# Kernel tuning notes

Measured on AMD Instinct MI355X. Metric: run time of the kernel, lower is better.

The kernel has to match this reference:

```python
import math
import jax, jax.numpy as jnp
import numpy as np

B, C_IN, C_OUT, K, STYLE_DIM, H, W = 8, 512, 512, 3, 512, 64, 64
EPS = 1e-8

def setup_inputs() -> dict:
    key = jax.random.key(0)
    k1, k2, k3, k4 = jax.random.split(key, 4)
    inp = {
        "input": jax.random.normal(k1, (B, C_IN, H, W), dtype=jnp.float32),
        "style": jax.random.normal(k2, (B, STYLE_DIM), dtype=jnp.float32),
        # learned params
        "weight": jax.random.normal(k3, (1, C_OUT, C_IN, K, K), dtype=jnp.float32),
        "mod_weight": jax.random.normal(k4, (C_IN, STYLE_DIM), dtype=jnp.float32),  # EqualLinear weight (lr_mul=1)
        "mod_bias": jnp.ones((C_IN,), dtype=jnp.float32),  # bias_init=1
    }
    return inp

def reference(input, style, weight, mod_weight, mod_bias):
    batch, in_ch, h, w = input.shape
    out_ch, ksize = weight.shape[1], weight.shape[-1]
    # EqualLinear modulation: scale = 1/sqrt(style_dim), lr_mul = 1
    mod_scale = 1.0 / math.sqrt(mod_weight.shape[1])
    s = style @ (mod_weight * mod_scale).T + mod_bias  # [B, C_in]
    # modulate weights per sample
    conv_scale = 1.0 / math.sqrt(in_ch * ksize * ksize)
    wmod = conv_scale * weight * s[:, None, :, None, None]  # [B, O, C, k, k]
    # demodulate
    demod = jax.lax.rsqrt(jnp.sum(wmod * wmod, axis=(2, 3, 4)) + EPS)  # [B, O]
    wmod = wmod * demod[:, :, None, None, None]
    # grouped conv with groups = batch
    wflat = wmod.reshape(batch * out_ch, in_ch, ksize, ksize)
    xflat = input.reshape(1, batch * in_ch, h, w)
    pad = ksize // 2
    out = jax.lax.conv_general_dilated(
        xflat, wflat,
        window_strides=(1, 1),
        padding=[(pad, pad), (pad, pad)],
        dimension_numbers=("NCHW", "OIHW", "NCHW"),
        feature_group_count=batch,
    )
    return out.reshape(batch, out_ch, h, w)
```

## Files before the change

### kernel.cpp

```cpp
#include <hip/hip_runtime.h>


typedef __bf16 bf16x8 __attribute__((ext_vector_type(8)));
typedef float f32x16 __attribute__((ext_vector_type(16)));

#define AS1 __attribute__((address_space(1)))
#define AS3 __attribute__((address_space(3)))
#define SB __builtin_amdgcn_sched_barrier(0)

__device__ __forceinline__ unsigned short f2bf(float f) {
  union { float f; unsigned int u; } v; v.f = f;
  unsigned int u = v.u;
  return (unsigned short)((u + 0x7fffu + ((u >> 16) & 1u)) >> 16);
}

__device__ __forceinline__ float dot8(float4 a0, float4 a1, float4 b0, float4 b1) {
  return a0.x*b0.x + a0.y*b0.y + a0.z*b0.z + a0.w*b0.w +
         a1.x*b1.x + a1.y*b1.y + a1.z*b1.z + a1.w*b1.w;
}

__global__ __launch_bounds__(256) void k_mod(
    const float* __restrict__ style, const float* __restrict__ mw,
    const float* __restrict__ mb, float* __restrict__ s,
    float* __restrict__ zp) {
  if (blockIdx.x == 0) {
    zp[threadIdx.x] = 0.f; zp[256 + threadIdx.x] = 0.f;
    zp[512 + threadIdx.x] = 0.f; zp[768 + threadIdx.x] = 0.f;
  }
  int wv = blockIdx.x * 4 + (threadIdx.x >> 6);
  int lane = threadIdx.x & 63;
  int t0 = wv * 4;
#pragma unroll
  for (int j = 0; j < 4; ++j) {
    int t = t0 + j, b = t >> 9, c = t & 511;
    const float4* mp = (const float4*)(mw + (size_t)c * 512 + lane * 8);
    const float4* sp = (const float4*)(style + (size_t)b * 512 + lane * 8);
    float p = dot8(mp[0], mp[1], sp[0], sp[1]);
#pragma unroll
    for (int off = 32; off; off >>= 1) p += __shfl_xor(p, off);
    if (lane == 0) s[t] = p * 0.04419417382415922f + mb[c];
  }
}

__global__ __launch_bounds__(256) void k_wprep(
    const float* __restrict__ w, float* __restrict__ wsq,
    unsigned short* __restrict__ wbf) {
  __shared__ float wl[4608];
  int o = blockIdx.x;
  int t = threadIdx.x;
  const float* wp = w + (size_t)o * 4608;
  for (int i = t; i < 4608; i += 256) wl[i] = wp[i];
  __syncthreads();
  int c0 = t * 2;
  float q0 = 0.f, q1 = 0.f;
  unsigned int rr[9];
#pragma unroll
  for (int k = 0; k < 9; ++k) {
    float v0 = wl[c0 * 9 + k], v1 = wl[c0 * 9 + 9 + k];
    q0 += v0 * v0; q1 += v1 * v1;
    rr[k] = (unsigned int)f2bf(v0) | ((unsigned int)f2bf(v1) << 16);
  }
  *(float2*)&wsq[o * 512 + c0] = make_float2(q0, q1);
#pragma unroll
  for (int k = 0; k < 9; ++k)
    *(unsigned int*)&wbf[((size_t)k * 512 + o) * 512 + c0] = rr[k];
}

__global__ __launch_bounds__(256) void k_scale(
    const float* __restrict__ wsq, const float* __restrict__ s,
    float* __restrict__ scale) {
  int o = blockIdx.x * 4 + (threadIdx.x >> 6);
  int lane = threadIdx.x & 63;
  const float4* wp = (const float4*)(wsq + (size_t)o * 512 + lane * 8);
  float4 w0 = wp[0], w1 = wp[1];
  const float cs = 0.014731391274719739f;
#pragma unroll
  for (int b = 0; b < 8; ++b) {
    const float4* sp = (const float4*)(s + (size_t)b * 512 + lane * 8);
    float4 s0 = sp[0], s1 = sp[1];
    s0.x *= s0.x; s0.y *= s0.y; s0.z *= s0.z; s0.w *= s0.w;
    s1.x *= s1.x; s1.y *= s1.y; s1.z *= s1.z; s1.w *= s1.w;
    float p = dot8(w0, w1, s0, s1);
#pragma unroll
    for (int off = 32; off; off >>= 1) p += __shfl_xor(p, off);
    if (lane == 0) scale[b * 512 + o] = cs * rsqrtf(cs * cs * p + 1e-8f);
  }
}

__global__ void k_xt(const float* __restrict__ x, const float* __restrict__ s,
                     unsigned short* __restrict__ xt) {
  __shared__ __align__(16) unsigned short tile[64 * 65 * 8];
  int bid = blockIdx.x;
  int b = bid >> 6, y = bid & 63;
  int t = threadIdx.x;
  int co = t >> 3, xo = t & 7;
  const float* xbase = x + ((size_t)(b * 512 + co * 8) * 64 + y) * 64 + xo * 8;
  float4 v[8][2];
#pragma unroll
  for (int j = 0; j < 8; ++j) {
    v[j][0] = *(const float4*)(xbase + (size_t)j * 4096);
    v[j][1] = *(const float4*)(xbase + (size_t)j * 4096 + 4);
  }
  float sv[8];
#pragma unroll
  for (int j = 0; j < 8; ++j) sv[j] = s[b * 512 + co * 8 + j];
#pragma unroll
  for (int k = 0; k < 8; ++k) {
    unsigned short r[8];
#pragma unroll
    for (int j = 0; j < 8; ++j) {
      float f = (k < 4) ? ((const float*)&v[j][0])[k & 3]
                        : ((const float*)&v[j][1])[k & 3];
      r[j] = f2bf(f * sv[j]);
    }
    int xr = xo * 8 + k;
    int unit = xr * 65 + (co ^ xr);
    *(ulonglong2*)&tile[unit * 8] = *(ulonglong2*)r;
  }
  __syncthreads();
  unsigned short* obase = xt + ((size_t)(b * 64 + y) * 64) * 512;
#pragma unroll
  for (int i = 0; i < 8; ++i) {
    int unit_o = i * 512 + t;
    int xr = unit_o >> 6, cor = unit_o & 63;
    int unit = xr * 65 + (cor ^ xr);
    *(ulonglong2*)&obase[(size_t)unit_o * 8] = *(const ulonglong2*)&tile[unit * 8];
  }
}

#define XISS 20
#define WOFF_US 10240
#define BUFU    28672

__global__ __launch_bounds__(512, 2) void k_conv(
    const unsigned short* __restrict__ xt, const unsigned short* __restrict__ wbf,
    const float* __restrict__ scale, const float* __restrict__ zp,
    float* __restrict__ out) {
  __shared__ __align__(16) unsigned short lds[2 * BUFU];

  int bid = blockIdx.x;
  int b = bid & 7;
  int rest = bid >> 3;
  int ob = rest & 3;
  int rest2 = rest >> 2;
  int yg = rest2 & 3;
  int xg = rest2 >> 2;

  int tid = threadIdx.x;
  int wid = tid >> 6;
  int wo = wid & 1, wyy = wid >> 1;
  int lane = tid & 63, ln31 = lane & 31, hi = lane >> 5;
  int cls = (wid >> 2) & 1;

  const char* srcp[7];
  const char* xglob = (const char*)(xt + (size_t)b * 64 * 64 * 512);
#pragma unroll
  for (int i = 0; i < 7; ++i) {
    int is = wid + i * 8;
    const char* p;
    if (is < XISS) {
      int e = is * 64 + lane;
      int chunk = e / 612;
      int rem = e - chunk * 612;
      int row = rem / 34;
      int xi = rem - row * 34;
      int y = yg * 16 + row - 1, x = xg * 32 + xi - 1;
      bool ok = (chunk < 2) && (y >= 0) && (y < 64) && (x >= 0) && (x < 64);
      p = ok ? xglob + 2 * ((y * 64 + x) * 512 + chunk * 8) : (const char*)zp;
    } else {
      int e2 = (is - XISS) * 64 + lane;
      int chunk = e2 / 1152;
      int rem = e2 - chunk * 1152;
      int tap = rem >> 7, o = rem & 127;
      p = (const char*)wbf + 2 * ((tap * 512 + ob * 128 + o) * 512 + chunk * 8);
    }
    srcp[i] = p;
  }

  f32x16 acc[8];
#pragma unroll
  for (int i = 0; i < 8; ++i)
    acc[i] = (f32x16){0,0,0,0,0,0,0,0,0,0,0,0,0,0,0,0};

  auto STAGE = [&](int bufu) {
#pragma unroll
    for (int i = 0; i < 7; ++i) {
      __builtin_amdgcn_global_load_lds(
          (const AS1 void*)srcp[i],
          (AS3 void*)&lds[bufu + (wid + i * 8) * 512], 16, 0, 0);
      srcp[i] += 32;
    }
  };

  auto LOADK = [&](const unsigned short* Xbp, const unsigned short* Abp,
                   int kx, bf16x8* bv, bf16x8* av) {
#pragma unroll
    for (int rr = 0; rr < 6; ++rr)
      bv[rr] = *(const bf16x8*)&Xbp[(rr * 34 + kx) * 8];
#pragma unroll
    for (int ky = 0; ky < 3; ++ky) {
      av[ky * 2]     = *(const bf16x8*)&Abp[(ky * 3 + kx) * 1024];
      av[ky * 2 + 1] = *(const bf16x8*)&Abp[(ky * 3 + kx) * 1024 + 256];
    }
  };

  auto MFK = [&](const bf16x8* bv, const bf16x8* av) {
    __builtin_amdgcn_s_setprio(1);
#pragma unroll
    for (int ky = 0; ky < 3; ++ky) {
#pragma unroll
      for (int ry = 0; ry < 4; ++ry) {
        acc[ry] = __builtin_amdgcn_mfma_f32_32x32x16_bf16(
            av[ky * 2], bv[ry + ky], acc[ry], 0, 0, 0);
        acc[4 + ry] = __builtin_amdgcn_mfma_f32_32x32x16_bf16(
            av[ky * 2 + 1], bv[ry + ky], acc[4 + ry], 0, 0, 0);
      }
    }
    __builtin_amdgcn_s_setprio(0);
  };

  auto COMPUTE = [&](const unsigned short* Xbp, const unsigned short* Abp) {
    bf16x8 b0[6], a0[6], b1[6], a1[6];
    if (cls == 0) {
      LOADK(Xbp, Abp, 0, b0, a0); SB;
      MFK(b0, a0); SB;
      LOADK(Xbp, Abp, 1, b1, a1); SB;
      MFK(b1, a1); SB;
      LOADK(Xbp, Abp, 2, b0, a0); SB;
      MFK(b0, a0);
    } else {
      LOADK(Xbp, Abp, 0, b0, a0);
      LOADK(Xbp, Abp, 1, b1, a1); SB;
      MFK(b0, a0); SB;
      LOADK(Xbp, Abp, 2, b0, a0); SB;
      MFK(b1, a1); SB;
      MFK(b0, a0);
    }
  };

  const unsigned short* Xb0 = &lds[(hi * 612 + wyy * 4 * 34 + ln31) * 8];
  const unsigned short* Ab0 = &lds[WOFF_US + (hi * 1152 + wo * 64 + ln31) * 8];
  const unsigned short* Xb1 = Xb0 + BUFU;
  const unsigned short* Ab1 = Ab0 + BUFU;

  STAGE(0);
  asm volatile("s_waitcnt vmcnt(0) lgkmcnt(0)" ::: "memory");
  __builtin_amdgcn_s_barrier();
  SB;

#pragma unroll 1
  for (int t = 0; t < 16; ++t) {
    STAGE(BUFU);
    COMPUTE(Xb0, Ab0);
    asm volatile("s_waitcnt vmcnt(0) lgkmcnt(0)" ::: "memory");
    __builtin_amdgcn_s_barrier();
    SB;
    if (t < 15) STAGE(0);
    COMPUTE(Xb1, Ab1);
    asm volatile("s_waitcnt vmcnt(0) lgkmcnt(0)" ::: "memory");
    __builtin_amdgcn_s_barrier();
    SB;
  }

  const float* scp = scale + b * 512 + ob * 128 + wo * 64;
  float* op = out + (((size_t)(b * 512 + ob * 128 + wo * 64) * 64) +
                     yg * 16 + wyy * 4) * 64 + xg * 32 + ln31;
#pragma unroll
  for (int oh = 0; oh < 2; ++oh) {
#pragma unroll
    for (int ry = 0; ry < 4; ++ry) {
      const f32x16& A = acc[oh * 4 + ry];
#pragma unroll
      for (int reg = 0; reg < 16; ++reg) {
        int orow = (reg & 3) + 8 * (reg >> 2) + hi * 4;
        int ol = oh * 32 + orow;
        op[(size_t)ol * 4096 + ry * 64] = A[reg] * scp[ol];
      }
    }
  }
}

extern "C" void kernel_launch(void* const* d_in, const int* in_sizes, int n_in,
                              void* d_out, int out_size, void* d_ws, size_t ws_size,
                              hipStream_t stream) {
  const float* x     = (const float*)d_in[0];
  const float* style = (const float*)d_in[1];
  const float* w     = (const float*)d_in[2];
  const float* mw    = (const float*)d_in[3];
  const float* mb    = (const float*)d_in[4];
  float* out = (float*)d_out;

  char* ws = (char*)d_ws;
  float* zp    = (float*)ws;
  float* s     = (float*)(ws + 4096);
  float* scale = (float*)(ws + 20480);
  float* wsq   = (float*)(ws + 36864);
  unsigned short* wbf = (unsigned short*)(ws + 1085440);
  unsigned short* xt  = (unsigned short*)(ws + 5804032);

  k_mod  <<<256,  256, 0, stream>>>(style, mw, mb, s, zp);
  k_wprep<<<512,  256, 0, stream>>>(w, wsq, wbf);
  k_scale<<<128,  256, 0, stream>>>(wsq, s, scale);
  k_xt   <<<512,  512, 0, stream>>>(x, s, xt);
  k_conv <<<256,  512, 0, stream>>>(xt, wbf, scale, zp, out);
}
```

Before: 184.7 us.

## Load conv weights directly from global into registers with a 4-deep LDS pipeline

```diff
diff --git a/kernel.cpp b/kernel.cpp
--- a/kernel.cpp
+++ b/kernel.cpp
@@ -44,7 +44,7 @@
 
 __global__ __launch_bounds__(256) void k_wprep(
     const float* __restrict__ w, float* __restrict__ wsq,
-    unsigned short* __restrict__ wbf) {
+    unsigned short* __restrict__ wbf2) {
   __shared__ float wl[4608];
   int o = blockIdx.x;
   int t = threadIdx.x;
@@ -62,8 +62,11 @@
   }
   *(float2*)&wsq[o * 512 + c0] = make_float2(q0, q1);
 #pragma unroll
-  for (int k = 0; k < 9; ++k)
-    *(unsigned int*)&wbf[((size_t)k * 512 + o) * 512 + c0] = rr[k];
+  for (int k = 0; k < 9; ++k) {
+    size_t idx = ((size_t)(k * 32 + (c0 >> 4)) * 512 + o) * 16 +
+                 ((c0 >> 3) & 1) * 8 + (c0 & 7);
+    *(unsigned int*)&wbf2[idx] = rr[k];
+  }
 }
 
 __global__ __launch_bounds__(256) void k_scale(
@@ -129,14 +132,13 @@
 }
 
 #define XISS 20
-#define WOFF_US 10240
-#define BUFU    28672
+#define BUFU  12288
 
 __global__ __launch_bounds__(512, 2) void k_conv(
-    const unsigned short* __restrict__ xt, const unsigned short* __restrict__ wbf,
+    const unsigned short* __restrict__ xt, const unsigned short* __restrict__ wbf2,
     const float* __restrict__ scale, const float* __restrict__ zp,
     float* __restrict__ out) {
-  __shared__ __align__(16) unsigned short lds[2 * BUFU];
+  __shared__ __align__(16) unsigned short lds[4 * BUFU];
 
   int bid = blockIdx.x;
   int b = bid & 7;
@@ -150,14 +152,13 @@
   int wid = tid >> 6;
   int wo = wid & 1, wyy = wid >> 1;
   int lane = tid & 63, ln31 = lane & 31, hi = lane >> 5;
-  int cls = (wid >> 2) & 1;
-
-  const char* srcp[7];
+
+  const char* srcp[3];
   const char* xglob = (const char*)(xt + (size_t)b * 64 * 64 * 512);
 #pragma unroll
-  for (int i = 0; i < 7; ++i) {
+  for (int i = 0; i < 3; ++i) {
     int is = wid + i * 8;
-    const char* p;
+    const char* p = (const char*)zp;
     if (is < XISS) {
       int e = is * 64 + lane;
       int chunk = e / 612;
@@ -166,45 +167,47 @@
       int xi = rem - row * 34;
       int y = yg * 16 + row - 1, x = xg * 32 + xi - 1;
       bool ok = (chunk < 2) && (y >= 0) && (y < 64) && (x >= 0) && (x < 64);
-      p = ok ? xglob + 2 * ((y * 64 + x) * 512 + chunk * 8) : (const char*)zp;
-    } else {
-      int e2 = (is - XISS) * 64 + lane;
-      int chunk = e2 / 1152;
-      int rem = e2 - chunk * 1152;
-      int tap = rem >> 7, o = rem & 127;
-      p = (const char*)wbf + 2 * ((tap * 512 + ob * 128 + o) * 512 + chunk * 8);
+      if (ok) p = xglob + 2 * ((y * 64 + x) * 512 + chunk * 8);
     }
     srcp[i] = p;
   }
+
+  const char* aw0 = (const char*)wbf2 +
+      2 * (((size_t)(ob * 128 + wo * 64 + ln31)) * 16 + hi * 8);
+  const char* aw1 = aw0 + 1024;
 
   f32x16 acc[8];
 #pragma unroll
   for (int i = 0; i < 8; ++i)
     acc[i] = (f32x16){0,0,0,0,0,0,0,0,0,0,0,0,0,0,0,0};
 
-  auto STAGE = [&](int bufu) {
-#pragma unroll
-    for (int i = 0; i < 7; ++i) {
+  auto STAGE = [&](int bufu, bool real) {
+#pragma unroll
+    for (int i = 0; i < 3; ++i) {
+      const char* src = real ? srcp[i] : (const char*)zp;
       __builtin_amdgcn_global_load_lds(
-          (const AS1 void*)srcp[i],
+          (const AS1 void*)src,
           (AS3 void*)&lds[bufu + (wid + i * 8) * 512], 16, 0, 0);
       srcp[i] += 32;
     }
   };
 
-  auto LOADK = [&](const unsigned short* Xbp, const unsigned short* Abp,
-                   int kx, bf16x8* bv, bf16x8* av) {
+  auto LOADA = [&](int kx, int aoff, bf16x8* A) {
+#pragma unroll
+    for (int ky = 0; ky < 3; ++ky) {
+      int tap = ky * 3 + kx;
+      A[ky * 2]     = *(const bf16x8*)(aw0 + (size_t)tap * 524288 + aoff);
+      A[ky * 2 + 1] = *(const bf16x8*)(aw1 + (size_t)tap * 524288 + aoff);
+    }
+  };
+
+  auto LOADB = [&](const unsigned short* Xbp, int kx, bf16x8* bv) {
 #pragma unroll
     for (int rr = 0; rr < 6; ++rr)
       bv[rr] = *(const bf16x8*)&Xbp[(rr * 34 + kx) * 8];
-#pragma unroll
-    for (int ky = 0; ky < 3; ++ky) {
-      av[ky * 2]     = *(const bf16x8*)&Abp[(ky * 3 + kx) * 1024];
-      av[ky * 2 + 1] = *(const bf16x8*)&Abp[(ky * 3 + kx) * 1024 + 256];
-    }
-  };
-
-  auto MFK = [&](const bf16x8* bv, const bf16x8* av) {
+  };
+
+  auto MFK = [&](const bf16x8* av, const bf16x8* bv) {
     __builtin_amdgcn_s_setprio(1);
 #pragma unroll
     for (int ky = 0; ky < 3; ++ky) {
@@ -219,47 +222,47 @@
     __builtin_amdgcn_s_setprio(0);
   };
 
-  auto COMPUTE = [&](const unsigned short* Xbp, const unsigned short* Abp) {
-    bf16x8 b0[6], a0[6], b1[6], a1[6];
-    if (cls == 0) {
-      LOADK(Xbp, Abp, 0, b0, a0); SB;
-      MFK(b0, a0); SB;
-      LOADK(Xbp, Abp, 1, b1, a1); SB;
-      MFK(b1, a1); SB;
-      LOADK(Xbp, Abp, 2, b0, a0); SB;
-      MFK(b0, a0);
-    } else {
-      LOADK(Xbp, Abp, 0, b0, a0);
-      LOADK(Xbp, Abp, 1, b1, a1); SB;
-      MFK(b0, a0); SB;
-      LOADK(Xbp, Abp, 2, b0, a0); SB;
-      MFK(b1, a1); SB;
-      MFK(b0, a0);
-    }
-  };
-
-  const unsigned short* Xb0 = &lds[(hi * 612 + wyy * 4 * 34 + ln31) * 8];
-  const unsigned short* Ab0 = &lds[WOFF_US + (hi * 1152 + wo * 64 + ln31) * 8];
-  const unsigned short* Xb1 = Xb0 + BUFU;
-  const unsigned short* Ab1 = Ab0 + BUFU;
-
-  STAGE(0);
-  asm volatile("s_waitcnt vmcnt(0) lgkmcnt(0)" ::: "memory");
+  auto PHASE = [&](const unsigned short* Xbp, int stageBufU, bool real,
+                   bf16x8* Su, bf16x8* Sl, int aoff) {
+    bf16x8 bv[6];
+    LOADB(Xbp, 0, bv);
+    STAGE(stageBufU, real);
+    LOADA(1, aoff, Sl);
+    MFK(Su, bv);
+    LOADB(Xbp, 1, bv);
+    LOADA(2, aoff, Su);
+    MFK(Sl, bv);
+    LOADB(Xbp, 2, bv);
+    LOADA(0, aoff + 16384, Sl);
+    MFK(Su, bv);
+    asm volatile("s_waitcnt vmcnt(9)" ::: "memory");
+    __builtin_amdgcn_s_barrier();
+    SB;
+  };
+
+  const unsigned short* Xw = &lds[(hi * 612 + wyy * 136 + ln31) * 8];
+  const unsigned short* Xq0 = Xw;
+  const unsigned short* Xq1 = Xw + BUFU;
+  const unsigned short* Xq2 = Xw + 2 * BUFU;
+  const unsigned short* Xq3 = Xw + 3 * BUFU;
+
+  bf16x8 SA[6], SB_[6];
+
+  STAGE(0, true);
+  STAGE(BUFU, true);
+  LOADA(0, 0, SA);
+  asm volatile("s_waitcnt vmcnt(9)" ::: "memory");
   __builtin_amdgcn_s_barrier();
   SB;
 
+  int aoff = 0;
 #pragma unroll 1
-  for (int t = 0; t < 16; ++t) {
-    STAGE(BUFU);
-    COMPUTE(Xb0, Ab0);
-    asm volatile("s_waitcnt vmcnt(0) lgkmcnt(0)" ::: "memory");
-    __builtin_amdgcn_s_barrier();
-    SB;
-    if (t < 15) STAGE(0);
-    COMPUTE(Xb1, Ab1);
-    asm volatile("s_waitcnt vmcnt(0) lgkmcnt(0)" ::: "memory");
-    __builtin_amdgcn_s_barrier();
-    SB;
+  for (int t4 = 0; t4 < 8; ++t4) {
+    bool r = (t4 < 7);
+    PHASE(Xq0, 2 * BUFU, true, SA, SB_, aoff); aoff += 16384;
+    PHASE(Xq1, 3 * BUFU, true, SB_, SA, aoff); aoff += 16384;
+    PHASE(Xq2, 0,        r,    SA, SB_, aoff); aoff += 16384;
+    PHASE(Xq3, 1 * BUFU, r,    SB_, SA, aoff); aoff += 16384;
   }
 
   const float* scp = scale + b * 512 + ob * 128 + wo * 64;
@@ -295,12 +298,12 @@
   float* s     = (float*)(ws + 4096);
   float* scale = (float*)(ws + 20480);
   float* wsq   = (float*)(ws + 36864);
-  unsigned short* wbf = (unsigned short*)(ws + 1085440);
-  unsigned short* xt  = (unsigned short*)(ws + 5804032);
+  unsigned short* wbf2 = (unsigned short*)(ws + 1085440);
+  unsigned short* xt   = (unsigned short*)(ws + 5804032);
 
   k_mod  <<<256,  256, 0, stream>>>(style, mw, mb, s, zp);
-  k_wprep<<<512,  256, 0, stream>>>(w, wsq, wbf);
+  k_wprep<<<512,  256, 0, stream>>>(w, wsq, wbf2);
   k_scale<<<128,  256, 0, stream>>>(wsq, s, scale);
   k_xt   <<<512,  512, 0, stream>>>(x, s, xt);
-  k_conv <<<256,  512, 0, stream>>>(xt, wbf, scale, zp, out);
-}
+  k_conv <<<256,  512, 0, stream>>>(xt, wbf2, scale, zp, out);
+}
```

Measured after the change: 178.0 us. -3.7%, faster.

## Restructure conv K-loop into triple-buffered X and double-buffered W pipeline

Applied to the files above, without the earlier changes.

```diff
diff --git a/kernel.cpp b/kernel.cpp
--- a/kernel.cpp
+++ b/kernel.cpp
@@ -128,15 +128,17 @@
   }
 }
 
-#define XISS 20
-#define WOFF_US 10240
-#define BUFU    28672
+#define XS0 0
+#define XS1 12288
+#define XS2 24576
+#define WS0 36864
+#define WS1 55296
 
 __global__ __launch_bounds__(512, 2) void k_conv(
     const unsigned short* __restrict__ xt, const unsigned short* __restrict__ wbf,
     const float* __restrict__ scale, const float* __restrict__ zp,
     float* __restrict__ out) {
-  __shared__ __align__(16) unsigned short lds[2 * BUFU];
+  __shared__ __align__(16) unsigned short lds[73728];
 
   int bid = blockIdx.x;
   int b = bid & 7;
@@ -150,31 +152,36 @@
   int wid = tid >> 6;
   int wo = wid & 1, wyy = wid >> 1;
   int lane = tid & 63, ln31 = lane & 31, hi = lane >> 5;
-  int cls = (wid >> 2) & 1;
-
-  const char* srcp[7];
+
+  const char* wsrc[5];
+  const char* xsrc[3];
   const char* xglob = (const char*)(xt + (size_t)b * 64 * 64 * 512);
 #pragma unroll
-  for (int i = 0; i < 7; ++i) {
-    int is = wid + i * 8;
-    const char* p;
-    if (is < XISS) {
-      int e = is * 64 + lane;
-      int chunk = e / 612;
-      int rem = e - chunk * 612;
-      int row = rem / 34;
-      int xi = rem - row * 34;
-      int y = yg * 16 + row - 1, x = xg * 32 + xi - 1;
-      bool ok = (chunk < 2) && (y >= 0) && (y < 64) && (x >= 0) && (x < 64);
-      p = ok ? xglob + 2 * ((y * 64 + x) * 512 + chunk * 8) : (const char*)zp;
-    } else {
-      int e2 = (is - XISS) * 64 + lane;
+  for (int j = 0; j < 5; ++j) {
+    int is2 = wid + 24 + j * 8;
+    if (is2 < 60) {
+      int e2 = (is2 - 24) * 64 + lane;
       int chunk = e2 / 1152;
       int rem = e2 - chunk * 1152;
       int tap = rem >> 7, o = rem & 127;
-      p = (const char*)wbf + 2 * ((tap * 512 + ob * 128 + o) * 512 + chunk * 8);
-    }
-    srcp[i] = p;
+      wsrc[j] = (const char*)wbf +
+                2 * ((tap * 512 + ob * 128 + o) * 512 + chunk * 8);
+    } else {
+      wsrc[j] = (const char*)zp;
+    }
+  }
+#pragma unroll
+  for (int j = 0; j < 3; ++j) {
+    int is = wid + j * 8;
+    int e = is * 64 + lane;
+    int chunk = e / 612;
+    int rem = e - chunk * 612;
+    int row = rem / 34;
+    int xi = rem - row * 34;
+    int y = yg * 16 + row - 1, x = xg * 32 + xi - 1;
+    bool ok = (chunk < 2) && (y >= 0) && (y < 64) && (x >= 0) && (x < 64);
+    xsrc[j] = ok ? xglob + 2 * ((y * 64 + x) * 512 + chunk * 8)
+                 : (const char*)zp;
   }
 
   f32x16 acc[8];
@@ -182,29 +189,42 @@
   for (int i = 0; i < 8; ++i)
     acc[i] = (f32x16){0,0,0,0,0,0,0,0,0,0,0,0,0,0,0,0};
 
-  auto STAGE = [&](int bufu) {
-#pragma unroll
-    for (int i = 0; i < 7; ++i) {
+  auto stageW = [&](int j, int wsb) {
+    int is2 = wid + 24 + j * 8;
+    if (is2 < 60) {
       __builtin_amdgcn_global_load_lds(
-          (const AS1 void*)srcp[i],
-          (AS3 void*)&lds[bufu + (wid + i * 8) * 512], 16, 0, 0);
-      srcp[i] += 32;
+          (const AS1 void*)wsrc[j],
+          (AS3 void*)&lds[wsb + (is2 - 24) * 512], 16, 0, 0);
+      wsrc[j] += 32;
     }
   };
-
-  auto LOADK = [&](const unsigned short* Xbp, const unsigned short* Abp,
-                   int kx, bf16x8* bv, bf16x8* av) {
+  auto stageX = [&](int j, int xsb) {
+    __builtin_amdgcn_global_load_lds(
+        (const AS1 void*)xsrc[j],
+        (AS3 void*)&lds[xsb + (wid + j * 8) * 512], 16, 0, 0);
+    xsrc[j] += 32;
+  };
+
+  auto PHASE = [&](const unsigned short* Xr, const unsigned short* Wr, int kx,
+                   int sk, int sbase, bool sg, int wait) {
+    bf16x8 bv[6], av[6];
 #pragma unroll
     for (int rr = 0; rr < 6; ++rr)
-      bv[rr] = *(const bf16x8*)&Xbp[(rr * 34 + kx) * 8];
+      bv[rr] = *(const bf16x8*)&Xr[(rr * 34 + kx) * 8];
 #pragma unroll
     for (int ky = 0; ky < 3; ++ky) {
-      av[ky * 2]     = *(const bf16x8*)&Abp[(ky * 3 + kx) * 1024];
-      av[ky * 2 + 1] = *(const bf16x8*)&Abp[(ky * 3 + kx) * 1024 + 256];
-    }
-  };
-
-  auto MFK = [&](const bf16x8* bv, const bf16x8* av) {
+      av[ky * 2]     = *(const bf16x8*)&Wr[(ky * 3 + kx) * 1024];
+      av[ky * 2 + 1] = *(const bf16x8*)&Wr[(ky * 3 + kx) * 1024 + 256];
+    }
+    if (sg) {
+      if (sk == 0) { stageW(0, sbase); stageW(1, sbase); stageW(2, sbase); }
+      if (sk == 1) { stageW(3, sbase); stageW(4, sbase); }
+      if (sk == 2) { stageX(0, sbase); stageX(1, sbase); stageX(2, sbase); }
+    }
+    SB;
+    __builtin_amdgcn_s_barrier();
+    asm volatile("s_waitcnt lgkmcnt(0)" ::: "memory");
+    SB;
     __builtin_amdgcn_s_setprio(1);
 #pragma unroll
     for (int ky = 0; ky < 3; ++ky) {
@@ -217,50 +237,49 @@
       }
     }
     __builtin_amdgcn_s_setprio(0);
+    SB;
+    if (wait == 1) asm volatile("s_waitcnt vmcnt(3)" ::: "memory");
+    if (wait == 2) asm volatile("s_waitcnt vmcnt(0)" ::: "memory");
+    __builtin_amdgcn_s_barrier();
+    SB;
   };
 
-  auto COMPUTE = [&](const unsigned short* Xbp, const unsigned short* Abp) {
-    bf16x8 b0[6], a0[6], b1[6], a1[6];
-    if (cls == 0) {
-      LOADK(Xbp, Abp, 0, b0, a0); SB;
-      MFK(b0, a0); SB;
-      LOADK(Xbp, Abp, 1, b1, a1); SB;
-      MFK(b1, a1); SB;
-      LOADK(Xbp, Abp, 2, b0, a0); SB;
-      MFK(b0, a0);
-    } else {
-      LOADK(Xbp, Abp, 0, b0, a0);
-      LOADK(Xbp, Abp, 1, b1, a1); SB;
-      MFK(b0, a0); SB;
-      LOADK(Xbp, Abp, 2, b0, a0); SB;
-      MFK(b1, a1); SB;
-      MFK(b0, a0);
-    }
+  auto TILE = [&](const unsigned short* Xr, const unsigned short* Wr,
+                  int wsb, int xsb, bool sgW, bool sgX, int wcode) {
+    PHASE(Xr, Wr, 0, 0, wsb, sgW, 0);
+    PHASE(Xr, Wr, 1, 1, wsb, sgW, 0);
+    PHASE(Xr, Wr, 2, 2, xsb, sgX, wcode);
   };
 
-  const unsigned short* Xb0 = &lds[(hi * 612 + wyy * 4 * 34 + ln31) * 8];
-  const unsigned short* Ab0 = &lds[WOFF_US + (hi * 1152 + wo * 64 + ln31) * 8];
-  const unsigned short* Xb1 = Xb0 + BUFU;
-  const unsigned short* Ab1 = Ab0 + BUFU;
-
-  STAGE(0);
-  asm volatile("s_waitcnt vmcnt(0) lgkmcnt(0)" ::: "memory");
+  int xoff = (hi * 612 + wyy * 136 + ln31) * 8;
+  int woff = (hi * 1152 + wo * 64 + ln31) * 8;
+  const unsigned short* Xr0 = &lds[XS0 + xoff];
+  const unsigned short* Xr1 = &lds[XS1 + xoff];
+  const unsigned short* Xr2 = &lds[XS2 + xoff];
+  const unsigned short* Wr0 = &lds[WS0 + woff];
+  const unsigned short* Wr1 = &lds[WS1 + woff];
+
+#pragma unroll
+  for (int j = 0; j < 5; ++j) stageW(j, WS0);
+#pragma unroll
+  for (int j = 0; j < 3; ++j) stageX(j, XS0);
+#pragma unroll
+  for (int j = 0; j < 3; ++j) stageX(j, XS1);
+  asm volatile("s_waitcnt vmcnt(3)" ::: "memory");
   __builtin_amdgcn_s_barrier();
   SB;
 
 #pragma unroll 1
-  for (int t = 0; t < 16; ++t) {
-    STAGE(BUFU);
-    COMPUTE(Xb0, Ab0);
-    asm volatile("s_waitcnt vmcnt(0) lgkmcnt(0)" ::: "memory");
-    __builtin_amdgcn_s_barrier();
-    SB;
-    if (t < 15) STAGE(0);
-    COMPUTE(Xb1, Ab1);
-    asm volatile("s_waitcnt vmcnt(0) lgkmcnt(0)" ::: "memory");
-    __builtin_amdgcn_s_barrier();
-    SB;
-  }
+  for (int tt = 0; tt < 30; tt += 6) {
+    TILE(Xr0, Wr0, WS1, XS2, true, true, 1);
+    TILE(Xr1, Wr1, WS0, XS0, true, true, 1);
+    TILE(Xr2, Wr0, WS1, XS1, true, true, 1);
+    TILE(Xr0, Wr1, WS0, XS2, true, true, 1);
+    TILE(Xr1, Wr0, WS1, XS0, true, true, 1);
+    TILE(Xr2, Wr1, WS0, XS1, true, true, 1);
+  }
+  TILE(Xr0, Wr0, WS1, XS2, true, false, 2);
+  TILE(Xr1, Wr1, WS0, XS0, false, false, 0);
 
   const float* scp = scale + b * 512 + ob * 128 + wo * 64;
   float* op = out + (((size_t)(b * 512 + ob * 128 + wo * 64) * 64) +
```

New measurement: 180.8 us. -2.1%, faster.
